# Optimization experiments

Hardware: AMD Instinct MI355X
Metric: run time of the kernel (lower is better)

## Reference

```python
import jax, jax.numpy as jnp
import numpy as np

L_MAX = 3


def setup_inputs() -> dict:
    key = jax.random.key(0)
    k1, k2, k3, k4 = jax.random.split(key, 4)
    B, V, P, Cin, R, Cout = 8, 4096, 32, 64, 2, 128
    N = (L_MAX + 1) ** 2  # 16 spherical-harmonic coeffs
    signal = jax.random.normal(k1, (B, V, Cin), dtype=jnp.float32)
    # gather_nd indices: [..., 0] = batch index, [..., 1] = point index
    bidx = jnp.broadcast_to(jnp.arange(B, dtype=jnp.int32)[:, None, None], (B, V, P))
    pidx = jax.random.randint(k2, (B, V, P), 0, V, dtype=jnp.int32)
    patches_idx = jnp.stack([bidx, pidx], axis=-1)
    conv_kernel = jax.random.normal(k3, (B, V, P, R, N), dtype=jnp.float32)
    kernel_weights = jax.random.normal(k4, (Cout, Cin, R, L_MAX + 1), dtype=jnp.float32)
    biases = jnp.zeros((Cout,), dtype=jnp.float32)
    return {"signal": signal, "patches_idx": patches_idx, "conv_kernel": conv_kernel,
            "kernel_weights": kernel_weights, "biases": biases}


def reference(signal, patches_idx, conv_kernel, kernel_weights, biases):
    l_max = kernel_weights.shape[-1] - 1
    # gather neighbor patches: [B, V, P, Cin]
    patches = signal[patches_idx[..., 0], patches_idx[..., 1]]
    # per-point conv over patch dim: [B, V, Cin, R, N]
    y = jnp.einsum('bvprn,bvpc->bvcrn', conv_kernel, patches)
    y = y * y
    # SH-invariant power per degree l: sum over the 2l+1 orders m
    blocks = []
    p = 0
    for l in range(l_max + 1):
        blocks.append(jnp.sum(y[..., p:p + 2 * l + 1], axis=-1))
        p += 2 * l + 1
    y = jnp.stack(blocks, axis=-1)  # [B, V, Cin, R, l_max+1]
    y = jnp.sqrt(jnp.maximum(y, 1e-4))
    out = jnp.einsum('ijrn,bvjrn->bvi', kernel_weights, y) + biases
    return jax.nn.relu(out)
```

## Files before the change

### kernel.cpp

```cpp
#include <hip/hip_runtime.h>
#include <cstddef>

namespace {

constexpr int kV = 4096;
constexpr int kBlocks = 8 * kV / 16;

typedef float f32x16 __attribute__((ext_vector_type(16)));
typedef float f32x4  __attribute__((ext_vector_type(4)));
typedef short bf16x8 __attribute__((ext_vector_type(8)));

union U8 { unsigned u[4]; uint4 q; bf16x8 v; };

__device__ inline unsigned pk_bf16(float a, float b) {
    unsigned ua = __float_as_uint(a);
    unsigned ub = __float_as_uint(b);
    ua = (ua + 0x7FFFu + ((ua >> 16) & 1u)) >> 16;
    ub = (ub + 0x7FFFu + ((ub >> 16) & 1u)) & 0xFFFF0000u;
    return ua | ub;
}

__global__ void convW(const float* __restrict__ W, unsigned* __restrict__ Wb) {
    const int i = blockIdx.x * 256 + threadIdx.x;
    const float2 w2 = ((const float2*)W)[i];
    Wb[i] = pk_bf16(w2.x, w2.y);
}

__global__ __launch_bounds__(256, 4)
void fused(const float* __restrict__ signal,
           const int* __restrict__ pidx_g,
           const float* __restrict__ ck_g,
           const unsigned short* __restrict__ Wb,
           const float* __restrict__ bias,
           float* __restrict__ out)
{
    __shared__ __align__(16) unsigned short zbf[16][520];
    __shared__ unsigned patchI[4][16][64];

    const int t = threadIdx.x;
    const int b = blockIdx.x >> 8;
    const int v_base = (blockIdx.x & 255) * 16;
    const int w    = t >> 6;
    const int lane = t & 63;
    const int n31  = lane & 31;
    const int h    = lane >> 5;

    unsigned (*pI)[64] = patchI[w];
    const float* sgb = signal + (size_t)b * kV * 64;

    for (int vg = 0; vg < 4; ++vg) {
        const int g = vg * 4 + w;
        const size_t bv = (size_t)b * kV + (v_base + g);
        const int vsv = pidx_g[(bv * 32 + n31) * 2 + 1];
        const float* ckv = ck_g + bv * 1024;

        __syncthreads();

        #pragma unroll
        for (int pp = 0; pp < 16; ++pp) {
            const int vs0 = __builtin_amdgcn_readlane(vsv, 2 * pp);
            const int vs1 = __builtin_amdgcn_readlane(vsv, 2 * pp + 1);
            const float s0 = sgb[(size_t)vs0 * 64 + lane];
            const float s1 = sgb[(size_t)vs1 * 64 + lane];
            pI[pp][lane] = pk_bf16(s0, s1);
        }

        U8 A0, A1;
        #pragma unroll
        for (int j2 = 0; j2 < 4; ++j2) {
            const int p0 = 8 * h + 2 * j2;
            A0.u[j2] = pk_bf16(ckv[(p0     ) * 32 + n31], ckv[(p0 +  1) * 32 + n31]);
            A1.u[j2] = pk_bf16(ckv[(p0 + 16) * 32 + n31], ckv[(p0 + 17) * 32 + n31]);
        }

        __syncthreads();

        U8 B00, B01, B10, B11;
        #pragma unroll
        for (int j2 = 0; j2 < 4; ++j2) {
            B00.u[j2] = pI[    4 * h + j2][n31];
            B01.u[j2] = pI[    4 * h + j2][n31 + 32];
            B10.u[j2] = pI[8 + 4 * h + j2][n31];
            B11.u[j2] = pI[8 + 4 * h + j2][n31 + 32];
        }

        f32x16 acc0, acc1;
        #pragma unroll
        for (int j = 0; j < 16; ++j) { acc0[j] = 0.f; acc1[j] = 0.f; }
        acc0 = __builtin_amdgcn_mfma_f32_32x32x16_bf16(A0.v, B00.v, acc0, 0, 0, 0);
        acc1 = __builtin_amdgcn_mfma_f32_32x32x16_bf16(A0.v, B01.v, acc1, 0, 0, 0);
        acc0 = __builtin_amdgcn_mfma_f32_32x32x16_bf16(A1.v, B10.v, acc0, 0, 0, 0);
        acc1 = __builtin_amdgcn_mfma_f32_32x32x16_bf16(A1.v, B11.v, acc1, 0, 0, 0);

        #pragma unroll
        for (int ct = 0; ct < 2; ++ct) {
            const f32x16 a = ct ? acc1 : acc0;
            float s[16];
            #pragma unroll
            for (int j = 0; j < 16; ++j) s[j] = a[j] * a[j];
            const float o00 = s[0], o10 = s[1] + s[2] + s[3];
            const float o20 = s[4], o30 = s[5] + s[6] + s[7];
            const float o01 = s[8], o11 = s[9] + s[10] + s[11];
            const float o21 = s[12], o31 = s[13] + s[14] + s[15];
            const float x0 = s[0] + s[1] + s[2] + s[3];
            const float x1 = s[4] + s[5] + s[6] + s[7];
            const float x2 = s[8] + s[9] + s[10] + s[11];
            const float x3 = s[12] + s[13] + s[14] + s[15];
            const float e0 = __shfl_xor(h ? x0 : o20, 32);
            const float e1 = __shfl_xor(h ? x1 : o30, 32);
            const float e2 = __shfl_xor(h ? x2 : o21, 32);
            const float e3 = __shfl_xor(h ? x3 : o31, 32);
            if (h == 0) {
                const float z00 = sqrtf(fmaxf(o00,      1e-4f));
                const float z10 = sqrtf(fmaxf(o10,      1e-4f));
                const float z20 = sqrtf(fmaxf(o20 + e0, 1e-4f));
                const float z30 = sqrtf(fmaxf(o30 + e1, 1e-4f));
                const float z01 = sqrtf(fmaxf(o01,      1e-4f));
                const float z11 = sqrtf(fmaxf(o11,      1e-4f));
                const float z21 = sqrtf(fmaxf(o21 + e2, 1e-4f));
                const float z31 = sqrtf(fmaxf(o31 + e3, 1e-4f));
                uint4 d;
                d.x = pk_bf16(z00, z10);
                d.y = pk_bf16(z20, z30);
                d.z = pk_bf16(z01, z11);
                d.w = pk_bf16(z21, z31);
                *(uint4*)&zbf[g][(n31 + 32 * ct) * 8] = d;
            }
        }
    }
    __syncthreads();

    const int m15 = lane & 15;
    const int q   = lane >> 4;
    f32x4 pa0, pa1;
    #pragma unroll
    for (int j = 0; j < 4; ++j) { pa0[j] = 0.f; pa1[j] = 0.f; }
    const int i0 = w * 32 + m15;
    const int i1 = w * 32 + 16 + m15;
    #pragma unroll 4
    for (int ks = 0; ks < 16; ++ks) {
        U8 Az, Bw0, Bw1;
        Az.q  = *(const uint4*)&zbf[m15][ks * 32 + q * 8];
        Bw0.q = *(const uint4*)&Wb[(size_t)i0 * 512 + ks * 32 + q * 8];
        Bw1.q = *(const uint4*)&Wb[(size_t)i1 * 512 + ks * 32 + q * 8];
        pa0 = __builtin_amdgcn_mfma_f32_16x16x32_bf16(Az.v, Bw0.v, pa0, 0, 0, 0);
        pa1 = __builtin_amdgcn_mfma_f32_16x16x32_bf16(Az.v, Bw1.v, pa1, 0, 0, 0);
    }
    const float bi0 = bias[i0], bi1 = bias[i1];
    #pragma unroll
    for (int reg = 0; reg < 4; ++reg) {
        const int g = q * 4 + reg;
        const size_t row = ((size_t)b * kV + v_base + g) * 128;
        out[row + i0] = fmaxf(pa0[reg] + bi0, 0.f);
        out[row + i1] = fmaxf(pa1[reg] + bi1, 0.f);
    }
}

}

extern "C" void kernel_launch(void* const* d_in, const int* in_sizes, int n_in,
                              void* d_out, int out_size, void* d_ws, size_t ws_size,
                              hipStream_t stream) {
    const float* signal = (const float*)d_in[0];
    const int*   pidx   = (const int*)d_in[1];
    const float* ck     = (const float*)d_in[2];
    const float* W      = (const float*)d_in[3];
    const float* bias   = (const float*)d_in[4];
    float* out = (float*)d_out;
    unsigned* Wb = (unsigned*)d_ws;

    convW<<<dim3(128), dim3(256), 0, stream>>>(W, Wb);
    fused<<<dim3(kBlocks), dim3(256), 0, stream>>>(
        signal, pidx, ck, (const unsigned short*)Wb, bias, out);
}
```

Baseline: 240.8 us.

## Software-pipeline gather and conv-kernel loads across vertex groups via register prefetch

Hoists the patch index loads for all four vertex groups, then prefetches the next group's gathered signal values and conv-kernel values into registers while the current group runs its MFMA and reduction. The aim is to hide global-load latency behind compute. This adds 48 live floats per thread, which may raise register use and lower occupancy under the 256x4 launch bound.

```diff
diff --git a/kernel.cpp b/kernel.cpp
--- a/kernel.cpp
+++ b/kernel.cpp
@@ -48,30 +48,54 @@
     unsigned (*pI)[64] = patchI[w];
     const float* sgb = signal + (size_t)b * kV * 64;
 
+    int vsl[4];
+    #pragma unroll
+    for (int vg = 0; vg < 4; ++vg)
+        vsl[vg] = pidx_g[((((size_t)b * kV + v_base + vg * 4 + w) * 32) + n31) * 2 + 1];
+
+    float sP[32];
+    float cP[16];
+
+    auto prefetch = [&](int vg) {
+        const size_t bv = (size_t)b * kV + (v_base + vg * 4 + w);
+        const float* ckv = ck_g + bv * 1024;
+        #pragma unroll
+        for (int pp = 0; pp < 16; ++pp) {
+            const int vs0 = __builtin_amdgcn_readlane(vsl[vg], 2 * pp);
+            const int vs1 = __builtin_amdgcn_readlane(vsl[vg], 2 * pp + 1);
+            sP[2 * pp    ] = sgb[(size_t)vs0 * 64 + lane];
+            sP[2 * pp + 1] = sgb[(size_t)vs1 * 64 + lane];
+        }
+        #pragma unroll
+        for (int j2 = 0; j2 < 4; ++j2) {
+            const int p0 = 8 * h + 2 * j2;
+            cP[4 * j2 + 0] = ckv[(p0     ) * 32 + n31];
+            cP[4 * j2 + 1] = ckv[(p0 +  1) * 32 + n31];
+            cP[4 * j2 + 2] = ckv[(p0 + 16) * 32 + n31];
+            cP[4 * j2 + 3] = ckv[(p0 + 17) * 32 + n31];
+        }
+    };
+
+    prefetch(0);
+
+    #pragma unroll
     for (int vg = 0; vg < 4; ++vg) {
         const int g = vg * 4 + w;
-        const size_t bv = (size_t)b * kV + (v_base + g);
-        const int vsv = pidx_g[(bv * 32 + n31) * 2 + 1];
-        const float* ckv = ck_g + bv * 1024;
 
         __syncthreads();
 
         #pragma unroll
-        for (int pp = 0; pp < 16; ++pp) {
-            const int vs0 = __builtin_amdgcn_readlane(vsv, 2 * pp);
-            const int vs1 = __builtin_amdgcn_readlane(vsv, 2 * pp + 1);
-            const float s0 = sgb[(size_t)vs0 * 64 + lane];
-            const float s1 = sgb[(size_t)vs1 * 64 + lane];
-            pI[pp][lane] = pk_bf16(s0, s1);
-        }
+        for (int pp = 0; pp < 16; ++pp)
+            pI[pp][lane] = pk_bf16(sP[2 * pp], sP[2 * pp + 1]);
 
         U8 A0, A1;
         #pragma unroll
         for (int j2 = 0; j2 < 4; ++j2) {
-            const int p0 = 8 * h + 2 * j2;
-            A0.u[j2] = pk_bf16(ckv[(p0     ) * 32 + n31], ckv[(p0 +  1) * 32 + n31]);
-            A1.u[j2] = pk_bf16(ckv[(p0 + 16) * 32 + n31], ckv[(p0 + 17) * 32 + n31]);
+            A0.u[j2] = pk_bf16(cP[4 * j2 + 0], cP[4 * j2 + 1]);
+            A1.u[j2] = pk_bf16(cP[4 * j2 + 2], cP[4 * j2 + 3]);
         }
+
+        if (vg < 3) prefetch(vg + 1);
 
         __syncthreads();
 
```

Result: no change. 238.7 us (-0.9%).

## Vectorize neighbor gather, prefetch indices, and drop block barriers in conv loop

Applied to the files above, without the earlier changes.

The signal gather changes from scalar per-lane loads to float4 loads. Each 16-lane group fetches one neighbor row, with indices broadcast by shuffle. The patch dimension is permuted consistently between the conv-kernel A operand and the LDS B operand. Point indices for all four vertex groups are loaded up front, and the loop is fully unrolled so more loads are in flight. Both __syncthreads in the loop are removed because each wave uses its own LDS region, which relies on wave-local ordering of the LDS write and read.

```diff
diff --git a/kernel.cpp b/kernel.cpp
--- a/kernel.cpp
+++ b/kernel.cpp
@@ -35,7 +35,7 @@
            float* __restrict__ out)
 {
     __shared__ __align__(16) unsigned short zbf[16][520];
-    __shared__ unsigned patchI[4][16][64];
+    __shared__ __align__(16) unsigned pS[4][16][64];
 
     const int t = threadIdx.x;
     const int b = blockIdx.x >> 8;
@@ -44,44 +44,63 @@
     const int lane = t & 63;
     const int n31  = lane & 31;
     const int h    = lane >> 5;
+    const int r4   = lane >> 4;
+    const int cq   = lane & 15;
 
-    unsigned (*pI)[64] = patchI[w];
+    unsigned (*pSw)[64] = pS[w];
     const float* sgb = signal + (size_t)b * kV * 64;
 
+    int vsl[4];
+    #pragma unroll
+    for (int vg = 0; vg < 4; ++vg)
+        vsl[vg] = pidx_g[((((size_t)b * kV + v_base + vg * 4 + w) * 32) + n31) * 2 + 1];
+
+    #pragma unroll
     for (int vg = 0; vg < 4; ++vg) {
         const int g = vg * 4 + w;
         const size_t bv = (size_t)b * kV + (v_base + g);
-        const int vsv = pidx_g[(bv * 32 + n31) * 2 + 1];
+        const int vsv = vsl[vg];
         const float* ckv = ck_g + bv * 1024;
 
-        __syncthreads();
+        float4 S[8];
+        #pragma unroll
+        for (int k = 0; k < 8; ++k) {
+            const int vs = __shfl(vsv, 4 * k + r4);
+            S[k] = *(const float4*)(sgb + (size_t)vs * 64 + cq * 4);
+        }
+        float cA[16];
+        #pragma unroll
+        for (int j2 = 0; j2 < 4; ++j2) {
+            cA[4 * j2 + 0] = ckv[(8 * j2 + h    ) * 32 + n31];
+            cA[4 * j2 + 1] = ckv[(8 * j2 + h + 4) * 32 + n31];
+            cA[4 * j2 + 2] = ckv[(8 * j2 + h + 2) * 32 + n31];
+            cA[4 * j2 + 3] = ckv[(8 * j2 + h + 6) * 32 + n31];
+        }
 
         #pragma unroll
-        for (int pp = 0; pp < 16; ++pp) {
-            const int vs0 = __builtin_amdgcn_readlane(vsv, 2 * pp);
-            const int vs1 = __builtin_amdgcn_readlane(vsv, 2 * pp + 1);
-            const float s0 = sgb[(size_t)vs0 * 64 + lane];
-            const float s1 = sgb[(size_t)vs1 * 64 + lane];
-            pI[pp][lane] = pk_bf16(s0, s1);
+        for (int m = 0; m < 4; ++m) {
+            uint4 d;
+            d.x = pk_bf16(S[2 * m].x, S[2 * m + 1].x);
+            d.y = pk_bf16(S[2 * m].y, S[2 * m + 1].y);
+            d.z = pk_bf16(S[2 * m].z, S[2 * m + 1].z);
+            d.w = pk_bf16(S[2 * m].w, S[2 * m + 1].w);
+            *(uint4*)&pSw[r4 * 4 + m][cq * 4] = d;
         }
 
         U8 A0, A1;
         #pragma unroll
         for (int j2 = 0; j2 < 4; ++j2) {
-            const int p0 = 8 * h + 2 * j2;
-            A0.u[j2] = pk_bf16(ckv[(p0     ) * 32 + n31], ckv[(p0 +  1) * 32 + n31]);
-            A1.u[j2] = pk_bf16(ckv[(p0 + 16) * 32 + n31], ckv[(p0 + 17) * 32 + n31]);
+            A0.u[j2] = pk_bf16(cA[4 * j2 + 0], cA[4 * j2 + 1]);
+            A1.u[j2] = pk_bf16(cA[4 * j2 + 2], cA[4 * j2 + 3]);
         }
-
-        __syncthreads();
 
         U8 B00, B01, B10, B11;
         #pragma unroll
         for (int j2 = 0; j2 < 4; ++j2) {
-            B00.u[j2] = pI[    4 * h + j2][n31];
-            B01.u[j2] = pI[    4 * h + j2][n31 + 32];
-            B10.u[j2] = pI[8 + 4 * h + j2][n31];
-            B11.u[j2] = pI[8 + 4 * h + j2][n31 + 32];
+            B00.u[j2] = pSw[    4 * h + j2][n31];
+            B01.u[j2] = pSw[    4 * h + j2][n31 + 32];
+            B10.u[j2] = pSw[8 + 4 * h + j2][n31];
+            B11.u[j2] = pSw[8 + 4 * h + j2][n31 + 32];
         }
 
         f32x16 acc0, acc1;
```

After: 239.1 us. No clear change (-0.7%).

## Split fused kernel into gather-conv phase and separate output GEMM via workspace

Applied to the files above, without the earlier changes.

Splits the single fused kernel into two. Phase1 runs one wave per point with no block-wide barriers and loads the conv kernel and gathered signal rows as coalesced float4, transposing through LDS. It writes the bf16 invariant features to a global workspace. Phase2 is a separate GEMM in which each wave computes all 128 output channels for 16 points, so each feature load is reused across eight MFMA tiles. This adds a global round trip for the intermediate z (about 32 MB) and an extra kernel launch.

```diff
diff --git a/kernel.cpp b/kernel.cpp
--- a/kernel.cpp
+++ b/kernel.cpp
@@ -4,7 +4,6 @@
 namespace {
 
 constexpr int kV = 4096;
-constexpr int kBlocks = 8 * kV / 16;
 
 typedef float f32x16 __attribute__((ext_vector_type(16)));
 typedef float f32x4  __attribute__((ext_vector_type(4)));
@@ -26,133 +25,149 @@
     Wb[i] = pk_bf16(w2.x, w2.y);
 }
 
-__global__ __launch_bounds__(256, 4)
-void fused(const float* __restrict__ signal,
-           const int* __restrict__ pidx_g,
-           const float* __restrict__ ck_g,
-           const unsigned short* __restrict__ Wb,
-           const float* __restrict__ bias,
-           float* __restrict__ out)
+__global__ __launch_bounds__(256, 5)
+void phase1(const float* __restrict__ signal,
+            const int* __restrict__ pidx_g,
+            const float* __restrict__ ck_g,
+            unsigned short* __restrict__ zG)
 {
-    __shared__ __align__(16) unsigned short zbf[16][520];
-    __shared__ unsigned patchI[4][16][64];
+    __shared__ float ckS[4][16][33];
+    __shared__ __align__(16) unsigned sgS[4][8][64];
 
     const int t = threadIdx.x;
-    const int b = blockIdx.x >> 8;
-    const int v_base = (blockIdx.x & 255) * 16;
-    const int w    = t >> 6;
-    const int lane = t & 63;
-    const int n31  = lane & 31;
-    const int h    = lane >> 5;
+    const int w = t >> 6, lane = t & 63;
+    const int n31 = lane & 31, h = lane >> 5;
+    const int r4 = lane >> 4, c16 = lane & 15;
 
-    unsigned (*pI)[64] = patchI[w];
-    const float* sgb = signal + (size_t)b * kV * 64;
+    const size_t bv = (size_t)blockIdx.x * 4 + w;
+    const int b = (int)(bv >> 12);
+    const float* sgb = signal + ((size_t)b << 12) * 64;
+    const float* ckv = ck_g + bv * 1024;
 
-    for (int vg = 0; vg < 4; ++vg) {
-        const int g = vg * 4 + w;
-        const size_t bv = (size_t)b * kV + (v_base + g);
-        const int vsv = pidx_g[(bv * 32 + n31) * 2 + 1];
-        const float* ckv = ck_g + bv * 1024;
+    const int vsv = pidx_g[(bv * 32 + n31) * 2 + 1];
 
-        __syncthreads();
+    float (*ck_s)[33] = ckS[w];
+    unsigned (*sg_s)[64] = sgS[w];
 
+    f32x16 acc0, acc1;
+    #pragma unroll
+    for (int j = 0; j < 16; ++j) { acc0[j] = 0.f; acc1[j] = 0.f; }
+
+    #pragma unroll
+    for (int h2 = 0; h2 < 2; ++h2) {
+        const float4* ckh = (const float4*)(ckv + h2 * 512);
+        const float4 C0 = ckh[lane * 2];
+        const float4 C1 = ckh[lane * 2 + 1];
+        float4 S[4];
         #pragma unroll
-        for (int pp = 0; pp < 16; ++pp) {
-            const int vs0 = __builtin_amdgcn_readlane(vsv, 2 * pp);
-            const int vs1 = __builtin_amdgcn_readlane(vsv, 2 * pp + 1);
-            const float s0 = sgb[(size_t)vs0 * 64 + lane];
-            const float s1 = sgb[(size_t)vs1 * 64 + lane];
-            pI[pp][lane] = pk_bf16(s0, s1);
+        for (int k = 0; k < 4; ++k) {
+            const int vs = __shfl(vsv, 16 * h2 + 4 * k + r4);
+            S[k] = *(const float4*)(sgb + (size_t)vs * 64 + c16 * 4);
         }
 
-        U8 A0, A1;
+        {
+            const int r = lane >> 2, cb = 8 * (lane & 3);
+            ck_s[r][cb + 0] = C0.x; ck_s[r][cb + 1] = C0.y;
+            ck_s[r][cb + 2] = C0.z; ck_s[r][cb + 3] = C0.w;
+            ck_s[r][cb + 4] = C1.x; ck_s[r][cb + 5] = C1.y;
+            ck_s[r][cb + 6] = C1.z; ck_s[r][cb + 7] = C1.w;
+        }
+        {
+            uint4 d0, d1;
+            d0.x = pk_bf16(S[0].x, S[1].x); d0.y = pk_bf16(S[0].y, S[1].y);
+            d0.z = pk_bf16(S[0].z, S[1].z); d0.w = pk_bf16(S[0].w, S[1].w);
+            d1.x = pk_bf16(S[2].x, S[3].x); d1.y = pk_bf16(S[2].y, S[3].y);
+            d1.z = pk_bf16(S[2].z, S[3].z); d1.w = pk_bf16(S[2].w, S[3].w);
+            *(uint4*)&sg_s[r4][c16 * 4]     = d0;
+            *(uint4*)&sg_s[4 + r4][c16 * 4] = d1;
+        }
+
+        U8 A, B0, B1;
         #pragma unroll
         for (int j2 = 0; j2 < 4; ++j2) {
-            const int p0 = 8 * h + 2 * j2;
-            A0.u[j2] = pk_bf16(ckv[(p0     ) * 32 + n31], ckv[(p0 +  1) * 32 + n31]);
-            A1.u[j2] = pk_bf16(ckv[(p0 + 16) * 32 + n31], ckv[(p0 + 17) * 32 + n31]);
+            const int rho = j2 + 8 * h;
+            A.u[j2]  = pk_bf16(ck_s[rho][n31], ck_s[rho + 4][n31]);
+            B0.u[j2] = sg_s[4 * h + j2][n31];
+            B1.u[j2] = sg_s[4 * h + j2][n31 + 32];
         }
+        acc0 = __builtin_amdgcn_mfma_f32_32x32x16_bf16(A.v, B0.v, acc0, 0, 0, 0);
+        acc1 = __builtin_amdgcn_mfma_f32_32x32x16_bf16(A.v, B1.v, acc1, 0, 0, 0);
+    }
 
-        __syncthreads();
-
-        U8 B00, B01, B10, B11;
+    #pragma unroll
+    for (int ct = 0; ct < 2; ++ct) {
+        const f32x16 a = ct ? acc1 : acc0;
+        float s[16];
         #pragma unroll
-        for (int j2 = 0; j2 < 4; ++j2) {
-            B00.u[j2] = pI[    4 * h + j2][n31];
-            B01.u[j2] = pI[    4 * h + j2][n31 + 32];
-            B10.u[j2] = pI[8 + 4 * h + j2][n31];
-            B11.u[j2] = pI[8 + 4 * h + j2][n31 + 32];
-        }
-
-        f32x16 acc0, acc1;
-        #pragma unroll
-        for (int j = 0; j < 16; ++j) { acc0[j] = 0.f; acc1[j] = 0.f; }
-        acc0 = __builtin_amdgcn_mfma_f32_32x32x16_bf16(A0.v, B00.v, acc0, 0, 0, 0);
-        acc1 = __builtin_amdgcn_mfma_f32_32x32x16_bf16(A0.v, B01.v, acc1, 0, 0, 0);
-        acc0 = __builtin_amdgcn_mfma_f32_32x32x16_bf16(A1.v, B10.v, acc0, 0, 0, 0);
-        acc1 = __builtin_amdgcn_mfma_f32_32x32x16_bf16(A1.v, B11.v, acc1, 0, 0, 0);
-
-        #pragma unroll
-        for (int ct = 0; ct < 2; ++ct) {
-            const f32x16 a = ct ? acc1 : acc0;
-            float s[16];
-            #pragma unroll
-            for (int j = 0; j < 16; ++j) s[j] = a[j] * a[j];
-            const float o00 = s[0], o10 = s[1] + s[2] + s[3];
-            const float o20 = s[4], o30 = s[5] + s[6] + s[7];
-            const float o01 = s[8], o11 = s[9] + s[10] + s[11];
-            const float o21 = s[12], o31 = s[13] + s[14] + s[15];
-            const float x0 = s[0] + s[1] + s[2] + s[3];
-            const float x1 = s[4] + s[5] + s[6] + s[7];
-            const float x2 = s[8] + s[9] + s[10] + s[11];
-            const float x3 = s[12] + s[13] + s[14] + s[15];
-            const float e0 = __shfl_xor(h ? x0 : o20, 32);
-            const float e1 = __shfl_xor(h ? x1 : o30, 32);
-            const float e2 = __shfl_xor(h ? x2 : o21, 32);
-            const float e3 = __shfl_xor(h ? x3 : o31, 32);
-            if (h == 0) {
-                const float z00 = sqrtf(fmaxf(o00,      1e-4f));
-                const float z10 = sqrtf(fmaxf(o10,      1e-4f));
-                const float z20 = sqrtf(fmaxf(o20 + e0, 1e-4f));
-                const float z30 = sqrtf(fmaxf(o30 + e1, 1e-4f));
-                const float z01 = sqrtf(fmaxf(o01,      1e-4f));
-                const float z11 = sqrtf(fmaxf(o11,      1e-4f));
-                const float z21 = sqrtf(fmaxf(o21 + e2, 1e-4f));
-                const float z31 = sqrtf(fmaxf(o31 + e3, 1e-4f));
-                uint4 d;
-                d.x = pk_bf16(z00, z10);
-                d.y = pk_bf16(z20, z30);
-                d.z = pk_bf16(z01, z11);
-                d.w = pk_bf16(z21, z31);
-                *(uint4*)&zbf[g][(n31 + 32 * ct) * 8] = d;
-            }
+        for (int j = 0; j < 16; ++j) s[j] = a[j] * a[j];
+        const float o00 = s[0], o10 = s[1] + s[2] + s[3];
+        const float o20 = s[4], o30 = s[5] + s[6] + s[7];
+        const float o01 = s[8], o11 = s[9] + s[10] + s[11];
+        const float o21 = s[12], o31 = s[13] + s[14] + s[15];
+        const float x0 = s[0] + s[1] + s[2] + s[3];
+        const float x1 = s[4] + s[5] + s[6] + s[7];
+        const float x2 = s[8] + s[9] + s[10] + s[11];
+        const float x3 = s[12] + s[13] + s[14] + s[15];
+        const float e0 = __shfl_xor(h ? x0 : o20, 32);
+        const float e1 = __shfl_xor(h ? x1 : o30, 32);
+        const float e2 = __shfl_xor(h ? x2 : o21, 32);
+        const float e3 = __shfl_xor(h ? x3 : o31, 32);
+        if (h == 0) {
+            const float z00 = sqrtf(fmaxf(o00,      1e-4f));
+            const float z10 = sqrtf(fmaxf(o10,      1e-4f));
+            const float z20 = sqrtf(fmaxf(o20 + e0, 1e-4f));
+            const float z30 = sqrtf(fmaxf(o30 + e1, 1e-4f));
+            const float z01 = sqrtf(fmaxf(o01,      1e-4f));
+            const float z11 = sqrtf(fmaxf(o11,      1e-4f));
+            const float z21 = sqrtf(fmaxf(o21 + e2, 1e-4f));
+            const float z31 = sqrtf(fmaxf(o31 + e3, 1e-4f));
+            uint4 d;
+            d.x = pk_bf16(z00, z10);
+            d.y = pk_bf16(z20, z30);
+            d.z = pk_bf16(z01, z11);
+            d.w = pk_bf16(z21, z31);
+            ((uint4*)(zG + bv * 512))[n31 + 32 * ct] = d;
         }
     }
-    __syncthreads();
+}
 
+__global__ __launch_bounds__(256, 4)
+void phase2(const unsigned short* __restrict__ zG,
+            const unsigned short* __restrict__ Wb,
+            const float* __restrict__ bias,
+            float* __restrict__ out)
+{
+    const int t = threadIdx.x;
+    const int w = t >> 6, lane = t & 63;
     const int m15 = lane & 15;
     const int q   = lane >> 4;
-    f32x4 pa0, pa1;
+    const int v0  = blockIdx.x * 64 + w * 16;
+
+    f32x4 acc[8];
     #pragma unroll
-    for (int j = 0; j < 4; ++j) { pa0[j] = 0.f; pa1[j] = 0.f; }
-    const int i0 = w * 32 + m15;
-    const int i1 = w * 32 + 16 + m15;
-    #pragma unroll 4
+    for (int nt = 0; nt < 8; ++nt)
+        #pragma unroll
+        for (int j = 0; j < 4; ++j) acc[nt][j] = 0.f;
+
+    #pragma unroll 2
     for (int ks = 0; ks < 16; ++ks) {
-        U8 Az, Bw0, Bw1;
-        Az.q  = *(const uint4*)&zbf[m15][ks * 32 + q * 8];
-        Bw0.q = *(const uint4*)&Wb[(size_t)i0 * 512 + ks * 32 + q * 8];
-        Bw1.q = *(const uint4*)&Wb[(size_t)i1 * 512 + ks * 32 + q * 8];
-        pa0 = __builtin_amdgcn_mfma_f32_16x16x32_bf16(Az.v, Bw0.v, pa0, 0, 0, 0);
-        pa1 = __builtin_amdgcn_mfma_f32_16x16x32_bf16(Az.v, Bw1.v, pa1, 0, 0, 0);
+        U8 Az;
+        Az.q = *(const uint4*)&zG[(size_t)(v0 + m15) * 512 + ks * 32 + q * 8];
+        #pragma unroll
+        for (int nt = 0; nt < 8; ++nt) {
+            U8 Bw;
+            Bw.q = *(const uint4*)&Wb[(size_t)(nt * 16 + m15) * 512 + ks * 32 + q * 8];
+            acc[nt] = __builtin_amdgcn_mfma_f32_16x16x32_bf16(Az.v, Bw.v, acc[nt], 0, 0, 0);
+        }
     }
-    const float bi0 = bias[i0], bi1 = bias[i1];
     #pragma unroll
-    for (int reg = 0; reg < 4; ++reg) {
-        const int g = q * 4 + reg;
-        const size_t row = ((size_t)b * kV + v_base + g) * 128;
-        out[row + i0] = fmaxf(pa0[reg] + bi0, 0.f);
-        out[row + i1] = fmaxf(pa1[reg] + bi1, 0.f);
+    for (int nt = 0; nt < 8; ++nt) {
+        const float bi = bias[nt * 16 + m15];
+        #pragma unroll
+        for (int reg = 0; reg < 4; ++reg) {
+            out[(size_t)(v0 + q * 4 + reg) * 128 + nt * 16 + m15] =
+                fmaxf(acc[nt][reg] + bi, 0.f);
+        }
     }
 }
 
@@ -167,9 +182,12 @@
     const float* W      = (const float*)d_in[3];
     const float* bias   = (const float*)d_in[4];
     float* out = (float*)d_out;
-    unsigned* Wb = (unsigned*)d_ws;
+
+    unsigned short* zG = (unsigned short*)d_ws;
+    unsigned* Wb = (unsigned*)((char*)d_ws + ((size_t)32 << 20));
 
     convW<<<dim3(128), dim3(256), 0, stream>>>(W, Wb);
-    fused<<<dim3(kBlocks), dim3(256), 0, stream>>>(
-        signal, pidx, ck, (const unsigned short*)Wb, bias, out);
+    phase1<<<dim3(8192), dim3(256), 0, stream>>>(signal, pidx, ck, zG);
+    phase2<<<dim3(512), dim3(256), 0, stream>>>(
+        zG, (const unsigned short*)Wb, bias, out);
 }
```

Result: slower. 263.0 us (+9.2%).
